# Optimization experiments

Hardware: AMD Instinct MI355X
Metric: run time of the kernel (lower is better)

Reference implementation:

```python
import jax, jax.numpy as jnp
import numpy as np

B, S, DM = 2, 2048, 2048
H, KV, HD = 16, 4, 128
THETA = 10000.0
EPS = 1e-6


def _rmsnorm(x, scale):
    # flax nnx.RMSNorm with dtype=float32: x / sqrt(mean(x^2)+eps) * scale
    var = jnp.mean(jnp.square(x.astype(jnp.float32)), axis=-1, keepdims=True)
    return (x.astype(jnp.float32) * jax.lax.rsqrt(var + EPS)) * scale


def _apply_rope(x, positions, base):
    # x: [B, S, heads, HD]; positions: [1, S]
    half = HD // 2
    fraction = 2.0 * jnp.arange(half, dtype=jnp.float32) / HD
    timescale = base ** fraction                              # [HD/2]
    sinusoid = positions[..., None].astype(jnp.float32) / timescale  # [1, S, HD/2]
    sinusoid = sinusoid[..., None, :]                         # [1, S, 1, HD/2]
    sin, cos = jnp.sin(sinusoid), jnp.cos(sinusoid)
    x1, x2 = x[..., :half], x[..., half:]
    return jnp.concatenate([x1 * cos - x2 * sin, x2 * cos + x1 * sin], axis=-1).astype(x.dtype)


def setup_inputs() -> dict:
    key = jax.random.key(0)
    ks = jax.random.split(key, 7)
    w = lambda k, shape: jax.random.normal(k, shape, jnp.float32) * 0.02
    return {
        "x": jax.random.normal(ks[0], (B, S, DM), jnp.float32),
        "wq": w(ks[1], (DM, H, HD)),
        "wk": w(ks[2], (DM, KV, HD)),
        "wv": w(ks[3], (DM, KV, HD)),
        "wo": w(ks[4], (H, HD, DM)),
        "q_scale": jnp.ones((HD,), jnp.float32),
        "k_scale": jnp.ones((HD,), jnp.float32),
    }


def reference(x, wq, wk, wv, wo, q_scale, k_scale):
    # QKV projections (LinearGeneral hidden -> (heads, head_dim))
    q = jnp.einsum("bsd,dhk->bshk", x, wq)   # [B,S,H,HD]
    k = jnp.einsum("bsd,dhk->bshk", x, wk)   # [B,S,KV,HD]
    v = jnp.einsum("bsd,dhk->bshk", x, wv)   # [B,S,KV,HD]
    # qk RMSNorm + cast back to compute dtype
    q = _rmsnorm(q, q_scale).astype(x.dtype)
    k = _rmsnorm(k, k_scale).astype(x.dtype)
    # RoPE
    positions = jnp.arange(S)[None, :]
    q = _apply_rope(q, positions, THETA)
    k = _apply_rope(k, positions, THETA)
    # GQA attention: group query heads per kv head instead of materializing repeat_kv
    G = H // KV
    qg = q.reshape(B, S, KV, G, HD) * (HD ** -0.5)
    scores = jnp.einsum("bqkgd,bskd->bkgqs", qg, k)           # [B,KV,G,S,S]
    causal = jnp.tril(jnp.ones((S, S), jnp.bool_))
    scores = jnp.where(causal, scores, jnp.finfo(scores.dtype).min)
    probs = jax.nn.softmax(scores, axis=-1)
    att = jnp.einsum("bkgqs,bskd->bqkgd", probs, v).reshape(B, S, H, HD)
    # output projection contracting (heads, head_dim)
    return jnp.einsum("bshd,hdo->bso", att, wo)
```

## Files before the change

### kernel.cpp

```cpp
#include <hip/hip_runtime.h>
#include <hip/hip_bf16.h>
#include <math.h>

typedef unsigned short u16;
typedef short short8 __attribute__((ext_vector_type(8)));
typedef float floatx4 __attribute__((ext_vector_type(4)));

#define B_   2
#define S_   2048
#define DM_  2048
#define H_   16
#define KVH_ 4
#define HD_  128

__device__ __forceinline__ float bf2f(u16 v) {
  union { unsigned int u; float f; } x; x.u = ((unsigned int)v) << 16; return x.f;
}
__device__ __forceinline__ u16 f2bf(float f) {
  union { float f; unsigned int u; } x; x.f = f;
  unsigned int u = x.u;
  u += 0x7FFFu + ((u >> 16) & 1u);
  return (u16)(u >> 16);
}

#define GLDS16(gp, lp) __builtin_amdgcn_global_load_lds( \
    (const __attribute__((address_space(1))) unsigned int*)(const void*)(gp), \
    (__attribute__((address_space(3))) unsigned int*)(void*)(lp), 16, 0, 0)

__global__ __launch_bounds__(256) void k_prep(
    const float* __restrict__ x, const float* __restrict__ wq,
    const float* __restrict__ wk, const float* __restrict__ wv,
    const float* __restrict__ wo,
    u16* __restrict__ x_bf, u16* __restrict__ wqkv_t, u16* __restrict__ wo_t)
{
  int bx = blockIdx.x;
  if (bx < 8192) {
    int i = bx * 256 + threadIdx.x;
    const float4 v = ((const float4*)x)[i];
    u16 o[4] = { f2bf(v.x), f2bf(v.y), f2bf(v.z), f2bf(v.w) };
    *(unsigned long long*)(x_bf + (size_t)i * 4) = *(unsigned long long*)o;
    return;
  }
  bx -= 8192;
  const float* src; u16* dst; int C, cb;
  if (bx < 4096)      { src = wq; dst = wqkv_t; C = 2048; cb = 64; }
  else if (bx < 5120) { bx -= 4096; src = wk; dst = wqkv_t + (size_t)2048 * 2048; C = 512; cb = 16; }
  else if (bx < 6144) { bx -= 5120; src = wv; dst = wqkv_t + (size_t)2560 * 2048; C = 512; cb = 16; }
  else                { bx -= 6144; src = wo; dst = wo_t; C = 2048; cb = 64; }
  const int R = 2048;
  int c0 = (bx % cb) * 32, r0 = (bx / cb) * 32;
  __shared__ float tile[32][33];
  int tx = threadIdx.x & 31, ty = threadIdx.x >> 5;
#pragma unroll
  for (int j = 0; j < 4; j++)
    tile[ty * 4 + j][tx] = src[(size_t)(r0 + ty * 4 + j) * C + c0 + tx];
  __syncthreads();
#pragma unroll
  for (int j = 0; j < 4; j++)
    dst[(size_t)(c0 + ty * 4 + j) * R + r0 + tx] = f2bf(tile[tx][ty * 4 + j]);
}

__global__ __launch_bounds__(256, 3) void k_gemm_bt(
    const u16* __restrict__ A, const u16* __restrict__ Bt,
    void* __restrict__ Cout, int M, int N, int K, int c_bf16)
{
  __shared__ u16 As[128 * 64];
  __shared__ u16 Bs[128 * 64];
  int tid = threadIdx.x;
  int lane = tid & 63;
  int quad = lane >> 4, l16 = lane & 15;
  int wid = tid >> 6;
  int m0 = blockIdx.y * 128, n0 = blockIdx.x * 128;
  int wm = (wid >> 1) * 64, wn = (wid & 1) * 64;

  floatx4 acc[4][4] = {};

  int srow = tid >> 3;
  int gjc0 = (tid & 7) ^ (srow & 7);
  const u16* Ap = A + (size_t)(m0 + srow) * K + gjc0 * 8;
  const u16* Bp = Bt + (size_t)(n0 + srow) * K + gjc0 * 8;
  u16* AsW = As + tid * 8;
  u16* BsW = Bs + tid * 8;

  for (int kt = 0; kt < K; kt += 64) {
    __syncthreads();
#pragma unroll
    for (int j = 0; j < 4; j++) {
      GLDS16(Ap + (size_t)(j * 32) * K, AsW + j * 2048);
      GLDS16(Bp + (size_t)(j * 32) * K, BsW + j * 2048);
    }
    Ap += 64; Bp += 64;
    __syncthreads();

#pragma unroll
    for (int ks = 0; ks < 2; ks++) {
      short8 af[4], bfv[4];
#pragma unroll
      for (int mi = 0; mi < 4; mi++) {
        int row = wm + mi * 16 + l16;
        af[mi] = *(const short8*)&As[row * 64 + (((ks * 4 + quad) ^ (row & 7)) * 8)];
      }
#pragma unroll
      for (int ni = 0; ni < 4; ni++) {
        int row = wn + ni * 16 + l16;
        bfv[ni] = *(const short8*)&Bs[row * 64 + (((ks * 4 + quad) ^ (row & 7)) * 8)];
      }
#pragma unroll
      for (int mi = 0; mi < 4; mi++)
#pragma unroll
        for (int ni = 0; ni < 4; ni++)
          acc[mi][ni] = __builtin_amdgcn_mfma_f32_16x16x32_bf16(
              af[mi], bfv[ni], acc[mi][ni], 0, 0, 0);
    }
  }

#pragma unroll
  for (int mi = 0; mi < 4; mi++)
#pragma unroll
    for (int ni = 0; ni < 4; ni++)
#pragma unroll
      for (int r = 0; r < 4; r++) {
        int row = m0 + wm + mi * 16 + quad * 4 + r;
        int col = n0 + wn + ni * 16 + l16;
        float v = acc[mi][ni][r];
        if (c_bf16) ((u16*)Cout)[(size_t)row * N + col] = f2bf(v);
        else        ((float*)Cout)[(size_t)row * N + col] = v;
      }
}

__global__ __launch_bounds__(256) void k_post(
    const u16* __restrict__ C1, const float* __restrict__ qs,
    const float* __restrict__ ks, u16* __restrict__ qr, u16* __restrict__ kr,
    u16* __restrict__ vt)
{
  int bx = blockIdx.x;
  if (bx < 4096) {
    int m = bx;
    int lane = threadIdx.x & 63, wid = threadIdx.x >> 6;
    int pos = m & (S_ - 1);
    float ts = powf(10000.0f, (float)lane * (1.0f / 64.0f));
    float ang = (float)pos / ts;
    float sn = sinf(ang), cs = cosf(ang);
    for (int r = wid; r < H_ + KVH_; r += 4) {
      bool isq = r < H_;
      const u16* src = C1 + (size_t)m * 3072 + (isq ? r * HD_ : DM_ + (r - H_) * HD_);
      float x1 = bf2f(src[lane]), x2 = bf2f(src[lane + 64]);
      float ss = x1 * x1 + x2 * x2;
#pragma unroll
      for (int d = 1; d < 64; d <<= 1) ss += __shfl_xor(ss, d);
      float rs = rsqrtf(ss * (1.0f / 128.0f) + 1e-6f);
      const float* sc = isq ? qs : ks;
      float y1 = x1 * rs * sc[lane];
      float y2 = x2 * rs * sc[lane + 64];
      float o1 = y1 * cs - y2 * sn;
      float o2 = y2 * cs + y1 * sn;
      if (isq) { o1 *= 0.088388347648318447f; o2 *= 0.088388347648318447f; }
      u16* dst = isq ? (qr + ((size_t)m * H_ + r) * HD_)
                     : (kr + ((size_t)m * KVH_ + (r - H_)) * HD_);
      dst[lane]      = f2bf(o1);
      dst[lane + 64] = f2bf(o2);
    }
    return;
  }
  bx -= 4096;
  int sx = bx & 63, rest = bx >> 6;
  int hy = rest & 3, bk = rest >> 2;
  int s0 = sx * 32, h0 = hy * 32;
  int b = bk >> 2, kv = bk & 3;
  __shared__ u16 tile[32][33];
  int tx = threadIdx.x & 31, ty = threadIdx.x >> 5;
#pragma unroll
  for (int j = 0; j < 4; j++)
    tile[ty * 4 + j][tx] =
        C1[(size_t)(b * S_ + s0 + ty * 4 + j) * 3072 + 2560 + kv * HD_ + h0 + tx];
  __syncthreads();
#pragma unroll
  for (int j = 0; j < 4; j++)
    vt[((size_t)bk * HD_ + h0 + ty * 4 + j) * S_ + s0 + tx] = tile[tx][ty * 4 + j];
}

__global__ __launch_bounds__(256, 2) void k_flash(
    const u16* __restrict__ qr, const u16* __restrict__ kr,
    const u16* __restrict__ vt, u16* __restrict__ att)
{
  __shared__ u16 smem[40960] __attribute__((aligned(16)));
  u16* Ps = smem + 32768;
  float* lpbuf = (float*)(smem + 32768);

  int tid = threadIdx.x, lane = tid & 63, wid = tid >> 6;
  int quad = lane >> 4, l16 = lane & 15;
  int rhalf = wid & 1;
  int shalf = wid >> 1;
  int bx = blockIdx.x;
  int it = 31 - (bx >> 5);
  int hb = bx & 31;
  int h = hb & 15, b = hb >> 4;
  int kvh = h >> 2;
  int q0 = it * 64;
  int NT = it + 1;

  short8 qf[2][4];
#pragma unroll
  for (int m = 0; m < 2; m++) {
    const u16* qb = qr + ((size_t)(b * S_ + q0 + rhalf * 32 + m * 16 + l16) * H_ + h) * HD_;
#pragma unroll
    for (int kk = 0; kk < 4; kk++)
      qf[m][kk] = *(const short8*)(qb + kk * 32 + quad * 8);
  }

  int gjk = (tid & 15) ^ ((tid >> 4) & 15);
  int gjv = (tid & 7) ^ ((tid >> 3) & 7);
  const u16* kp = kr + ((size_t)(b * S_ + (tid >> 4)) * KVH_ + kvh) * HD_ + gjk * 8;
  const u16* vp = vt + ((size_t)(b * KVH_ + kvh) * HD_ + (tid >> 3)) * S_ + gjv * 8;

#pragma unroll
  for (int j = 0; j < 4; j++) {
    GLDS16(kp + (size_t)(j * 16) * KVH_ * HD_, smem + (size_t)(j * 256 + tid) * 8);
    GLDS16(vp + (size_t)(j * 32) * S_,         smem + 16384 + (size_t)(j * 256 + tid) * 8);
  }
  kp += (size_t)64 * KVH_ * HD_;
  vp += 64;
  __syncthreads();

  floatx4 accO[2][8] = {};
  float lp[2][4] = {};
  u16* PsW = Ps + wid * 2048;

  const float LOG2E = 1.4426950408889634f;
  const float MBIAS = -12.5f * 1.4426950408889634f;
  int qmax = q0 + rhalf * 32 + 31;

  for (int kt = 0; kt < NT; kt++) {
    if (kt + 1 < NT) {
      u16* KD = smem + (size_t)((kt + 1) & 1) * 8192;
      u16* VD = smem + 16384 + (size_t)((kt + 1) & 1) * 8192;
#pragma unroll
      for (int j = 0; j < 4; j++) {
        GLDS16(kp + (size_t)(j * 16) * KVH_ * HD_, KD + (size_t)(j * 256 + tid) * 8);
        GLDS16(vp + (size_t)(j * 32) * S_,         VD + (size_t)(j * 256 + tid) * 8);
      }
      kp += (size_t)64 * KVH_ * HD_;
      vp += 64;
    }

    int k0 = kt * 64;
    int s0w = k0 + shalf * 32;
    if (s0w <= qmax) {
      const u16* KsC = smem + (size_t)(kt & 1) * 8192;
      const u16* VtC = smem + 16384 + (size_t)(kt & 1) * 8192;

      floatx4 sacc[2][2] = {};
      __builtin_amdgcn_s_setprio(1);
#pragma unroll
      for (int kk = 0; kk < 4; kk++) {
        short8 kf[2];
#pragma unroll
        for (int nt = 0; nt < 2; nt++) {
          int row = shalf * 32 + nt * 16 + l16;
          kf[nt] = *(const short8*)&KsC[row * 128 + (((kk * 4 + quad) ^ (row & 15)) * 8)];
        }
#pragma unroll
        for (int nt = 0; nt < 2; nt++) {
          sacc[0][nt] = __builtin_amdgcn_mfma_f32_16x16x32_bf16(qf[0][kk], kf[nt], sacc[0][nt], 0, 0, 0);
          sacc[1][nt] = __builtin_amdgcn_mfma_f32_16x16x32_bf16(qf[1][kk], kf[nt], sacc[1][nt], 0, 0, 0);
        }
      }
      __builtin_amdgcn_s_setprio(0);

      bool diag = (s0w + 31 > q0 + rhalf * 32);
#pragma unroll
      for (int m = 0; m < 2; m++)
#pragma unroll
        for (int r = 0; r < 4; r++) {
          int prow = m * 16 + quad * 4 + r;
          int qrow = q0 + rhalf * 32 + prow;
          float rsum = 0.f;
#pragma unroll
          for (int nt = 0; nt < 2; nt++) {
            float p = __builtin_amdgcn_exp2f(fmaf(sacc[m][nt][r], LOG2E, MBIAS));
            if (diag && (s0w + nt * 16 + l16) > qrow) p = 0.f;
            rsum += p;
            int chunk = nt * 2 + (l16 >> 3);
            PsW[prow * 64 + ((chunk ^ (prow & 7)) * 8) + (l16 & 7)] = f2bf(p);
          }
          lp[m][r] += rsum;
        }

      __builtin_amdgcn_s_setprio(1);
      short8 pf[2];
#pragma unroll
      for (int m = 0; m < 2; m++) {
        int prow = m * 16 + l16;
        pf[m] = *(const short8*)&PsW[prow * 64 + ((quad ^ (prow & 7)) * 8)];
      }
#pragma unroll
      for (int ht = 0; ht < 8; ht++) {
        int row = ht * 16 + l16;
        short8 vf = *(const short8*)&VtC[row * 64 + (((shalf * 4 + quad) ^ (row & 7)) * 8)];
        accO[0][ht] = __builtin_amdgcn_mfma_f32_16x16x32_bf16(pf[0], vf, accO[0][ht], 0, 0, 0);
        accO[1][ht] = __builtin_amdgcn_mfma_f32_16x16x32_bf16(pf[1], vf, accO[1][ht], 0, 0, 0);
      }
      __builtin_amdgcn_s_setprio(0);
    }
    __syncthreads();
  }

#pragma unroll
  for (int m = 0; m < 2; m++)
#pragma unroll
    for (int r = 0; r < 4; r++) {
#pragma unroll
      for (int d = 1; d < 16; d <<= 1) lp[m][r] += __shfl_xor(lp[m][r], d);
    }

  floatx4* xch = (floatx4*)(void*)smem;
  if (wid >= 2) {
    floatx4* dst = xch + ((wid & 1) * 1024 + lane * 16);
#pragma unroll
    for (int m = 0; m < 2; m++)
#pragma unroll
      for (int ht = 0; ht < 8; ht++)
        dst[(m * 8 + ht + lane) & 15] = accO[m][ht];
    if (l16 == 0) {
#pragma unroll
      for (int m = 0; m < 2; m++)
#pragma unroll
        for (int r = 0; r < 4; r++)
          lpbuf[(wid & 1) * 32 + m * 16 + quad * 4 + r] = lp[m][r];
    }
  }
  __syncthreads();
  if (wid < 2) {
    floatx4* src = xch + (wid * 1024 + lane * 16);
    float inv[2][4];
#pragma unroll
    for (int m = 0; m < 2; m++)
#pragma unroll
      for (int ht = 0; ht < 8; ht++)
        accO[m][ht] += src[(m * 8 + ht + lane) & 15];
#pragma unroll
    for (int m = 0; m < 2; m++)
#pragma unroll
      for (int r = 0; r < 4; r++)
        inv[m][r] = 1.0f / (lp[m][r] + lpbuf[wid * 32 + m * 16 + quad * 4 + r]);
#pragma unroll
    for (int m = 0; m < 2; m++)
#pragma unroll
      for (int ht = 0; ht < 8; ht++)
#pragma unroll
        for (int r = 0; r < 4; r++) {
          int row = q0 + wid * 32 + m * 16 + quad * 4 + r;
          att[((size_t)(b * S_ + row) * H_ + h) * HD_ + ht * 16 + l16] =
              f2bf(accO[m][ht][r] * inv[m][r]);
        }
  }
}

extern "C" void kernel_launch(void* const* d_in, const int* in_sizes, int n_in,
                              void* d_out, int out_size, void* d_ws, size_t ws_size,
                              hipStream_t stream)
{
  const float* x  = (const float*)d_in[0];
  const float* wq = (const float*)d_in[1];
  const float* wk = (const float*)d_in[2];
  const float* wv = (const float*)d_in[3];
  const float* wo = (const float*)d_in[4];
  const float* qs = (const float*)d_in[5];
  const float* ks = (const float*)d_in[6];

  char* ws = (char*)d_ws;
  size_t off = 0;
  u16* x_bf   = (u16*)(ws + off); off += (size_t)4096 * 2048 * 2;
  u16* wqkv_t = (u16*)(ws + off); off += (size_t)3072 * 2048 * 2;
  u16* wo_t   = (u16*)(ws + off); off += (size_t)2048 * 2048 * 2;
  u16* C1     = (u16*)(ws + off); off += (size_t)4096 * 3072 * 2;
  u16* q_rope = (u16*)(ws + off); off += (size_t)4096 * 16 * 128 * 2;
  u16* k_rope = (u16*)(ws + off); off += (size_t)4096 * 4 * 128 * 2;
  u16* vt     = (u16*)(ws + off); off += (size_t)8 * 128 * 2048 * 2;
  u16* att    = (u16*)(ws + off); off += (size_t)4096 * 2048 * 2;

  k_prep<<<dim3(18432), 256, 0, stream>>>(x, wq, wk, wv, wo, x_bf, wqkv_t, wo_t);

  k_gemm_bt<<<dim3(24, 32), 256, 0, stream>>>(x_bf, wqkv_t, C1, 4096, 3072, 2048, 1);

  k_post<<<dim3(6144), 256, 0, stream>>>(C1, qs, ks, q_rope, k_rope, vt);

  k_flash<<<dim3(1024), 256, 0, stream>>>(q_rope, k_rope, vt, att);

  k_gemm_bt<<<dim3(16, 32), 256, 0, stream>>>(att, wo_t, d_out, 4096, 2048, 2048, 0);

  (void)in_sizes; (void)n_in; (void)out_size; (void)ws_size;
}
```

Measured before the change: 294.9 us.

## Fuse QK RMSNorm and RoPE into QKV GEMM epilogue with precomputed RoPE table

Adds a specialised QKV GEMM whose epilogue applies RMSNorm, RoPE and the query scale directly on the accumulators for Q and K tiles. Partner halves are exchanged through shared memory so each row can be normalised and rotated in place. Only V columns are still written to C1, and a slimmer kernel transposes them. The cos/sin values now come from a table built in the prep kernel instead of per-row powf/sin/cos. This removes the C1 round trip for Q/K and the separate post-processing pass, at the cost of extra syncs and scattered 2-byte stores in the GEMM epilogue.

```diff
diff --git a/kernel.cpp b/kernel.cpp
--- a/kernel.cpp
+++ b/kernel.cpp
@@ -31,9 +31,19 @@
     const float* __restrict__ x, const float* __restrict__ wq,
     const float* __restrict__ wk, const float* __restrict__ wv,
     const float* __restrict__ wo,
-    u16* __restrict__ x_bf, u16* __restrict__ wqkv_t, u16* __restrict__ wo_t)
+    u16* __restrict__ x_bf, u16* __restrict__ wqkv_t, u16* __restrict__ wo_t,
+    float2* __restrict__ rope_tab)
 {
   int bx = blockIdx.x;
+  if (bx >= 18432) {
+    int idx = (bx - 18432) * 256 + threadIdx.x;
+    int pos = idx >> 6;
+    float fi = (float)(idx & 63);
+    float ts = powf(10000.0f, fi * (1.0f / 64.0f));
+    float ang = (float)pos / ts;
+    rope_tab[idx] = make_float2(cosf(ang), sinf(ang));
+    return;
+  }
   if (bx < 8192) {
     int i = bx * 256 + threadIdx.x;
     const float4 v = ((const float4*)x)[i];
@@ -128,41 +138,137 @@
       }
 }
 
-__global__ __launch_bounds__(256) void k_post(
-    const u16* __restrict__ C1, const float* __restrict__ qs,
-    const float* __restrict__ ks, u16* __restrict__ qr, u16* __restrict__ kr,
-    u16* __restrict__ vt)
+__global__ __launch_bounds__(256, 3) void k_gemm_qkv(
+    const u16* __restrict__ A, const u16* __restrict__ Bt,
+    const float* __restrict__ qs, const float* __restrict__ ks,
+    const float2* __restrict__ tab,
+    u16* __restrict__ C1, u16* __restrict__ qr, u16* __restrict__ kr)
+{
+  const int K = 2048, N = 3072;
+  __shared__ u16 smem[16384] __attribute__((aligned(16)));
+  u16* As = smem;
+  u16* Bs = smem + 8192;
+  float* exch = (float*)smem;
+
+  int tid = threadIdx.x;
+  int lane = tid & 63;
+  int quad = lane >> 4, l16 = lane & 15;
+  int wid = tid >> 6;
+  int m0 = blockIdx.y * 128, n0 = blockIdx.x * 128;
+  int wm = (wid >> 1) * 64, wn = (wid & 1) * 64;
+
+  floatx4 acc[4][4] = {};
+
+  int srow = tid >> 3;
+  int gjc0 = (tid & 7) ^ (srow & 7);
+  const u16* Ap = A + (size_t)(m0 + srow) * K + gjc0 * 8;
+  const u16* Bp = Bt + (size_t)(n0 + srow) * K + gjc0 * 8;
+  u16* AsW = As + tid * 8;
+  u16* BsW = Bs + tid * 8;
+
+  for (int kt = 0; kt < K; kt += 64) {
+    __syncthreads();
+#pragma unroll
+    for (int j = 0; j < 4; j++) {
+      GLDS16(Ap + (size_t)(j * 32) * K, AsW + j * 2048);
+      GLDS16(Bp + (size_t)(j * 32) * K, BsW + j * 2048);
+    }
+    Ap += 64; Bp += 64;
+    __syncthreads();
+
+#pragma unroll
+    for (int ks = 0; ks < 2; ks++) {
+      short8 af[4], bfv[4];
+#pragma unroll
+      for (int mi = 0; mi < 4; mi++) {
+        int row = wm + mi * 16 + l16;
+        af[mi] = *(const short8*)&As[row * 64 + (((ks * 4 + quad) ^ (row & 7)) * 8)];
+      }
+#pragma unroll
+      for (int ni = 0; ni < 4; ni++) {
+        int row = wn + ni * 16 + l16;
+        bfv[ni] = *(const short8*)&Bs[row * 64 + (((ks * 4 + quad) ^ (row & 7)) * 8)];
+      }
+#pragma unroll
+      for (int mi = 0; mi < 4; mi++)
+#pragma unroll
+        for (int ni = 0; ni < 4; ni++)
+          acc[mi][ni] = __builtin_amdgcn_mfma_f32_16x16x32_bf16(
+              af[mi], bfv[ni], acc[mi][ni], 0, 0, 0);
+    }
+  }
+
+  int nt = blockIdx.x;
+  if (nt >= 20) {
+#pragma unroll
+    for (int mi = 0; mi < 4; mi++)
+#pragma unroll
+      for (int ni = 0; ni < 4; ni++)
+#pragma unroll
+        for (int r = 0; r < 4; r++) {
+          int row = m0 + wm + mi * 16 + quad * 4 + r;
+          int col = n0 + wn + ni * 16 + l16;
+          C1[(size_t)row * N + col] = f2bf(acc[mi][ni][r]);
+        }
+    return;
+  }
+
+  bool isq = nt < 16;
+  const float* scp = isq ? qs : ks;
+  float sc_own[4], sc_par[4];
+#pragma unroll
+  for (int ni = 0; ni < 4; ni++) {
+    sc_own[ni] = scp[wn + ni * 16 + l16];
+    sc_par[ni] = scp[(wn ^ 64) + ni * 16 + l16];
+  }
+  float ssign = (wn == 0) ? -1.0f : 1.0f;
+
+#pragma unroll
+  for (int mi = 0; mi < 4; mi++) {
+    __syncthreads();
+#pragma unroll
+    for (int ni = 0; ni < 4; ni++)
+#pragma unroll
+      for (int r = 0; r < 4; r++)
+        exch[(ni * 4 + r) * 256 + wid * 64 + lane] = acc[mi][ni][r];
+    __syncthreads();
+    float part[4][4];
+#pragma unroll
+    for (int ni = 0; ni < 4; ni++)
+#pragma unroll
+      for (int r = 0; r < 4; r++)
+        part[ni][r] = exch[(ni * 4 + r) * 256 + (wid ^ 1) * 64 + lane];
+
+#pragma unroll
+    for (int r = 0; r < 4; r++) {
+      float ss = 0.f;
+#pragma unroll
+      for (int ni = 0; ni < 4; ni++)
+        ss += acc[mi][ni][r] * acc[mi][ni][r] + part[ni][r] * part[ni][r];
+#pragma unroll
+      for (int d = 1; d < 16; d <<= 1) ss += __shfl_xor(ss, d);
+      float rs = rsqrtf(ss * (1.0f / 128.0f) + 1e-6f);
+      int row = m0 + wm + mi * 16 + quad * 4 + r;
+      int pos = row & (S_ - 1);
+#pragma unroll
+      for (int ni = 0; ni < 4; ni++) {
+        float2 cs = tab[pos * 64 + ni * 16 + l16];
+        float yo = acc[mi][ni][r] * rs * sc_own[ni];
+        float yp = part[ni][r] * rs * sc_par[ni];
+        float o = fmaf(ssign * yp, cs.y, yo * cs.x);
+        if (isq) o *= 0.088388347648318447f;
+        int d = wn + ni * 16 + l16;
+        if (isq) qr[((size_t)row * H_ + nt) * HD_ + d] = f2bf(o);
+        else     kr[((size_t)row * KVH_ + (nt - 16)) * HD_ + d] = f2bf(o);
+      }
+    }
+  }
+}
+
+__global__ __launch_bounds__(256) void k_vt(
+    const u16* __restrict__ C1, u16* __restrict__ vt)
 {
   int bx = blockIdx.x;
-  if (bx < 4096) {
-    int m = bx;
-    int lane = threadIdx.x & 63, wid = threadIdx.x >> 6;
-    int pos = m & (S_ - 1);
-    float ts = powf(10000.0f, (float)lane * (1.0f / 64.0f));
-    float ang = (float)pos / ts;
-    float sn = sinf(ang), cs = cosf(ang);
-    for (int r = wid; r < H_ + KVH_; r += 4) {
-      bool isq = r < H_;
-      const u16* src = C1 + (size_t)m * 3072 + (isq ? r * HD_ : DM_ + (r - H_) * HD_);
-      float x1 = bf2f(src[lane]), x2 = bf2f(src[lane + 64]);
-      float ss = x1 * x1 + x2 * x2;
-#pragma unroll
-      for (int d = 1; d < 64; d <<= 1) ss += __shfl_xor(ss, d);
-      float rs = rsqrtf(ss * (1.0f / 128.0f) + 1e-6f);
-      const float* sc = isq ? qs : ks;
-      float y1 = x1 * rs * sc[lane];
-      float y2 = x2 * rs * sc[lane + 64];
-      float o1 = y1 * cs - y2 * sn;
-      float o2 = y2 * cs + y1 * sn;
-      if (isq) { o1 *= 0.088388347648318447f; o2 *= 0.088388347648318447f; }
-      u16* dst = isq ? (qr + ((size_t)m * H_ + r) * HD_)
-                     : (kr + ((size_t)m * KVH_ + (r - H_)) * HD_);
-      dst[lane]      = f2bf(o1);
-      dst[lane + 64] = f2bf(o2);
-    }
-    return;
-  }
-  bx -= 4096;
   int sx = bx & 63, rest = bx >> 6;
   int hy = rest & 3, bk = rest >> 2;
   int s0 = sx * 32, h0 = hy * 32;
@@ -378,12 +484,14 @@
   u16* k_rope = (u16*)(ws + off); off += (size_t)4096 * 4 * 128 * 2;
   u16* vt     = (u16*)(ws + off); off += (size_t)8 * 128 * 2048 * 2;
   u16* att    = (u16*)(ws + off); off += (size_t)4096 * 2048 * 2;
-
-  k_prep<<<dim3(18432), 256, 0, stream>>>(x, wq, wk, wv, wo, x_bf, wqkv_t, wo_t);
-
-  k_gemm_bt<<<dim3(24, 32), 256, 0, stream>>>(x_bf, wqkv_t, C1, 4096, 3072, 2048, 1);
-
-  k_post<<<dim3(6144), 256, 0, stream>>>(C1, qs, ks, q_rope, k_rope, vt);
+  float2* rope_tab = (float2*)(ws + off); off += (size_t)2048 * 64 * 8;
+
+  k_prep<<<dim3(18944), 256, 0, stream>>>(x, wq, wk, wv, wo, x_bf, wqkv_t, wo_t, rope_tab);
+
+  k_gemm_qkv<<<dim3(24, 32), 256, 0, stream>>>(x_bf, wqkv_t, qs, ks, rope_tab,
+                                               C1, q_rope, k_rope);
+
+  k_vt<<<dim3(2048), 256, 0, stream>>>(C1, vt);
 
   k_flash<<<dim3(1024), 256, 0, stream>>>(q_rope, k_rope, vt, att);
 
```

After: 298.0 us. Within noise of the previous version (+1.0%).
